# Optimization experiments

Hardware: AMD Instinct MI355X
Metric: run time of the kernel (lower is better)

## Reference

```python
import jax, jax.numpy as jnp
import numpy as np

N_NODES = 100000


def setup_inputs() -> dict:
    key = jax.random.key(0)
    ks = jax.random.split(key, 7)
    feats = jax.random.normal(ks[0], (N_NODES, 128), dtype=jnp.float32)
    src = jax.random.randint(ks[1], (1000000,), 0, N_NODES)
    dst = jax.random.randint(ks[2], (1000000,), 0, N_NODES)
    W1 = jax.random.normal(ks[3], (128, 128), dtype=jnp.float32) * (1.0 / np.sqrt(128))
    b1 = jnp.zeros((128,), dtype=jnp.float32)
    W2 = jax.random.normal(ks[4], (128, 40), dtype=jnp.float32) * (1.0 / np.sqrt(128))
    b2 = jnp.zeros((40,), dtype=jnp.float32)
    return {"feats": feats, "src": src, "dst": dst, "W1": W1, "b1": b1, "W2": W2, "b2": b2}


def _sage_gcn_layer(h, src, dst, deg, W, b):
    # DGL SAGEConv aggregator_type='gcn':
    #   neigh = sum over in-edges of src features; h = (neigh + h_self) / (in_deg + 1); out = h @ W + b
    neigh = jax.ops.segment_sum(h[src], dst, num_segments=N_NODES)  # [N, d]
    agg = (neigh + h) / (deg[:, None] + 1.0)
    return agg @ W + b


def reference(feats, src, dst, W1, b1, W2, b2):
    deg = jax.ops.segment_sum(jnp.ones_like(dst, dtype=feats.dtype), dst, num_segments=N_NODES)
    h1 = jax.nn.relu(_sage_gcn_layer(feats, src, dst, deg, W1, b1))  # dropout = identity (eval)
    h2 = _sage_gcn_layer(h1, src, dst, deg, W2, b2)
    # original returns (h_list, h); h_list = [h1, h2], final h = h2
    return (h1, h2)
```

## Files before the change

kernel.cpp:

```cpp
#include <hip/hip_runtime.h>

static inline int ceil_div(int a, int b){ return (a+b-1)/b; }

__global__ __launch_bounds__(256) void k_hist(const int* __restrict__ dst, int E, int* __restrict__ cnt){
  int e = blockIdx.x*256 + threadIdx.x;
  if (e < E) atomicAdd(&cnt[dst[e]], 1);
}

__global__ __launch_bounds__(256) void k_scan_a(const int* __restrict__ cnt, int N, int* __restrict__ bsum){
  __shared__ int s[256];
  int t = threadIdx.x;
  int i0 = blockIdx.x*512 + 2*t;
  int a = (i0   < N) ? cnt[i0]   : 0;
  int b = (i0+1 < N) ? cnt[i0+1] : 0;
  s[t] = a + b;
  __syncthreads();
  for (int off=128; off>0; off>>=1){ if (t<off) s[t]+=s[t+off]; __syncthreads(); }
  if (t==0) bsum[blockIdx.x] = s[0];
}

__global__ __launch_bounds__(256) void k_scan_b(int* __restrict__ bsum, int nb){
  __shared__ int s[256];
  int t = threadIdx.x;
  int v0=0,v1=0,v2=0,v3=0;
  int i0 = t*4;
  if (i0   < nb) v0 = bsum[i0];
  if (i0+1 < nb) v1 = bsum[i0+1];
  if (i0+2 < nb) v2 = bsum[i0+2];
  if (i0+3 < nb) v3 = bsum[i0+3];
  int tsum = v0+v1+v2+v3;
  s[t] = tsum;
  __syncthreads();
  for (int off=1; off<256; off<<=1){
    int v = (t>=off) ? s[t-off] : 0;
    __syncthreads();
    s[t] += v;
    __syncthreads();
  }
  int excl = s[t] - tsum;
  if (i0   < nb) bsum[i0]   = excl;
  if (i0+1 < nb) bsum[i0+1] = excl + v0;
  if (i0+2 < nb) bsum[i0+2] = excl + v0 + v1;
  if (i0+3 < nb) bsum[i0+3] = excl + v0 + v1 + v2;
}

__global__ __launch_bounds__(256) void k_scan_c(const int* __restrict__ cnt, int N,
                                                const int* __restrict__ bsum, int* __restrict__ offs){
  __shared__ int s[256];
  int t = threadIdx.x;
  int i0 = blockIdx.x*512 + 2*t;
  int a = (i0   < N) ? cnt[i0]   : 0;
  int b = (i0+1 < N) ? cnt[i0+1] : 0;
  int tsum = a+b;
  s[t] = tsum;
  __syncthreads();
  for (int off=1; off<256; off<<=1){
    int v = (t>=off) ? s[t-off] : 0;
    __syncthreads();
    s[t] += v;
    __syncthreads();
  }
  int excl = s[t] - tsum + bsum[blockIdx.x];
  if (i0   < N) offs[i0]   = excl;
  if (i0+1 < N) offs[i0+1] = excl + a;
}

__global__ __launch_bounds__(256) void k_place(const int* __restrict__ src, const int* __restrict__ dst, int E,
                                               int* __restrict__ offs, int* __restrict__ ss){
  int e = blockIdx.x*256 + threadIdx.x;
  if (e < E){
    int d = dst[e];
    int p = atomicAdd(&offs[d], 1);
    ss[p] = src[e];
  }
}

__global__ __launch_bounds__(256) void k_agg1(const float* __restrict__ feats,
    const int* __restrict__ ss, const int* __restrict__ offs, const int* __restrict__ cnt,
    float* __restrict__ aggout, int N){
  int w = (int)((blockIdx.x*256u + threadIdx.x) >> 6);
  int lane = threadIdx.x & 63;
  if (w >= N) return;
  int c   = __builtin_amdgcn_readfirstlane(cnt[w]);
  int beg = __builtin_amdgcn_readfirstlane(offs[w]) - c;
  const float4* f4 = (const float4*)feats;
  int half = lane >> 5;
  int qc   = lane & 31;
  float4 acc = make_float4(0.f,0.f,0.f,0.f);
  int i = 0;
  for (; i+8 <= c; i += 8){
    int i0 = ss[beg+i  +half];
    int i1 = ss[beg+i+2+half];
    int i2 = ss[beg+i+4+half];
    int i3 = ss[beg+i+6+half];
    float4 a = f4[(size_t)i0*32 + qc];
    float4 b = f4[(size_t)i1*32 + qc];
    float4 cc= f4[(size_t)i2*32 + qc];
    float4 d = f4[(size_t)i3*32 + qc];
    acc.x += (a.x + b.x) + (cc.x + d.x);
    acc.y += (a.y + b.y) + (cc.y + d.y);
    acc.z += (a.z + b.z) + (cc.z + d.z);
    acc.w += (a.w + b.w) + (cc.w + d.w);
  }
  for (; i+2 <= c; i += 2){
    int i0 = ss[beg+i+half];
    float4 a = f4[(size_t)i0*32 + qc];
    acc.x += a.x; acc.y += a.y; acc.z += a.z; acc.w += a.w;
  }
  acc.x += __shfl_down(acc.x, 32, 64);
  acc.y += __shfl_down(acc.y, 32, 64);
  acc.z += __shfl_down(acc.z, 32, 64);
  acc.w += __shfl_down(acc.w, 32, 64);
  if (lane < 32){
    if (i < c){
      int i0 = ss[beg+i];
      float4 a = f4[(size_t)i0*32 + qc];
      acc.x += a.x; acc.y += a.y; acc.z += a.z; acc.w += a.w;
    }
    float4 s = f4[(size_t)w*32 + qc];
    float inv = 1.0f / (float)(c + 1);
    float4 o;
    o.x = (acc.x + s.x) * inv;
    o.y = (acc.y + s.y) * inv;
    o.z = (acc.z + s.z) * inv;
    o.w = (acc.w + s.w) * inv;
    ((float4*)aggout)[(size_t)w*32 + qc] = o;
  }
}

__global__ __launch_bounds__(256) void k_gemm12(float* __restrict__ h1,
    const float* __restrict__ W1, const float* __restrict__ b1,
    const float* __restrict__ W2, float* __restrict__ t1, int N){
  __shared__ float sA[64*132];
  __shared__ float sW[5120];
  int t = threadIdx.x;
  int r0 = blockIdx.x*64;
  for (int it=0; it<8; ++it){
    int flat = it*1024 + t*4;
    int r = flat>>7, d = flat&127;
    float4 v = make_float4(0.f,0.f,0.f,0.f);
    if (r0+r < N) v = *(const float4*)(h1 + (size_t)(r0+r)*128 + d);
    *(float4*)&sA[r*132 + d] = v;
  }
  int rg = t>>4, cg = t&15;
  float acc[4][8];
#pragma unroll
  for (int i=0;i<4;++i)
#pragma unroll
    for (int j=0;j<8;++j) acc[i][j]=0.f;

  for (int kc=0; kc<4; ++kc){
    __syncthreads();
#pragma unroll
    for (int it=0; it<4; ++it){
      int flat = it*1024 + t*4;
      *(float4*)&sW[flat] = *(const float4*)(W1 + kc*4096 + flat);
    }
    __syncthreads();
#pragma unroll 4
    for (int dd=0; dd<32; ++dd){
      int d = kc*32 + dd;
      float4 w0 = *(const float4*)&sW[dd*128 + cg*4];
      float4 w1 = *(const float4*)&sW[dd*128 + 64 + cg*4];
      float a0 = sA[(rg   )*132 + d];
      float a1 = sA[(rg+16)*132 + d];
      float a2 = sA[(rg+32)*132 + d];
      float a3 = sA[(rg+48)*132 + d];
      acc[0][0]+=a0*w0.x; acc[0][1]+=a0*w0.y; acc[0][2]+=a0*w0.z; acc[0][3]+=a0*w0.w;
      acc[0][4]+=a0*w1.x; acc[0][5]+=a0*w1.y; acc[0][6]+=a0*w1.z; acc[0][7]+=a0*w1.w;
      acc[1][0]+=a1*w0.x; acc[1][1]+=a1*w0.y; acc[1][2]+=a1*w0.z; acc[1][3]+=a1*w0.w;
      acc[1][4]+=a1*w1.x; acc[1][5]+=a1*w1.y; acc[1][6]+=a1*w1.z; acc[1][7]+=a1*w1.w;
      acc[2][0]+=a2*w0.x; acc[2][1]+=a2*w0.y; acc[2][2]+=a2*w0.z; acc[2][3]+=a2*w0.w;
      acc[2][4]+=a2*w1.x; acc[2][5]+=a2*w1.y; acc[2][6]+=a2*w1.z; acc[2][7]+=a2*w1.w;
      acc[3][0]+=a3*w0.x; acc[3][1]+=a3*w0.y; acc[3][2]+=a3*w0.z; acc[3][3]+=a3*w0.w;
      acc[3][4]+=a3*w1.x; acc[3][5]+=a3*w1.y; acc[3][6]+=a3*w1.z; acc[3][7]+=a3*w1.w;
    }
  }
  __syncthreads();

  float4 bb0 = *(const float4*)(b1 + cg*4);
  float4 bb1 = *(const float4*)(b1 + 64 + cg*4);
#pragma unroll
  for (int i=0;i<4;++i){
    int rr = rg + i*16;
    int r  = r0 + rr;
    float4 o0, o1;
    o0.x = fmaxf(acc[i][0]+bb0.x, 0.f); o0.y = fmaxf(acc[i][1]+bb0.y, 0.f);
    o0.z = fmaxf(acc[i][2]+bb0.z, 0.f); o0.w = fmaxf(acc[i][3]+bb0.w, 0.f);
    o1.x = fmaxf(acc[i][4]+bb1.x, 0.f); o1.y = fmaxf(acc[i][5]+bb1.y, 0.f);
    o1.z = fmaxf(acc[i][6]+bb1.z, 0.f); o1.w = fmaxf(acc[i][7]+bb1.w, 0.f);
    *(float4*)&sA[rr*132 + cg*4]      = o0;
    *(float4*)&sA[rr*132 + 64 + cg*4] = o1;
    if (r < N){
      *(float4*)(h1 + (size_t)r*128 + cg*4)      = o0;
      *(float4*)(h1 + (size_t)r*128 + 64 + cg*4) = o1;
    }
  }
#pragma unroll
  for (int it=0; it<5; ++it){
    int flat = it*1024 + t*4;
    *(float4*)&sW[flat] = *(const float4*)(W2 + flat);
  }
  __syncthreads();

  int rg2 = t>>3, cg2 = t&7;
  float a2c[2][5];
#pragma unroll
  for (int i=0;i<2;++i)
#pragma unroll
    for (int j=0;j<5;++j) a2c[i][j]=0.f;
#pragma unroll 4
  for (int d=0; d<128; ++d){
    float a0 = sA[(rg2   )*132 + d];
    float a1 = sA[(rg2+32)*132 + d];
#pragma unroll
    for (int jj=0;jj<5;++jj){
      float wv = sW[d*40 + cg2 + 8*jj];
      a2c[0][jj] += a0*wv;
      a2c[1][jj] += a1*wv;
    }
  }
#pragma unroll
  for (int i=0;i<2;++i){
    int r = r0 + rg2 + i*32;
    if (r < N){
#pragma unroll
      for (int jj=0;jj<5;++jj) t1[(size_t)r*40 + cg2 + 8*jj] = a2c[i][jj];
    }
  }
}

__global__ __launch_bounds__(256) void k_agg2(const float* __restrict__ t1,
    const int* __restrict__ ss, const int* __restrict__ offs, const int* __restrict__ cnt,
    const float* __restrict__ b2, float* __restrict__ h2, int N){
  int w = (int)((blockIdx.x*256u + threadIdx.x) >> 6);
  int lane = threadIdx.x & 63;
  if (w >= N) return;
  int c   = __builtin_amdgcn_readfirstlane(cnt[w]);
  int beg = __builtin_amdgcn_readfirstlane(offs[w]) - c;
  int l = (lane < 40) ? lane : 0;
  float acc = t1[(size_t)w*40 + l];
  int i = 0;
  for (; i+4 <= c; i += 4){
    int s0 = ss[beg+i], s1 = ss[beg+i+1], s2 = ss[beg+i+2], s3 = ss[beg+i+3];
    float a = t1[(size_t)s0*40 + l];
    float b = t1[(size_t)s1*40 + l];
    float cc= t1[(size_t)s2*40 + l];
    float d = t1[(size_t)s3*40 + l];
    acc += (a + b) + (cc + d);
  }
  for (; i < c; ++i) acc += t1[(size_t)ss[beg+i]*40 + l];
  float inv = 1.0f / (float)(c + 1);
  if (lane < 40) h2[(size_t)w*40 + lane] = acc*inv + b2[lane];
}

extern "C" void kernel_launch(void* const* d_in, const int* in_sizes, int n_in,
                              void* d_out, int out_size, void* d_ws, size_t ws_size,
                              hipStream_t stream){
  const float* feats = (const float*)d_in[0];
  const int*   src   = (const int*)d_in[1];
  const int*   dst   = (const int*)d_in[2];
  const float* W1    = (const float*)d_in[3];
  const float* b1    = (const float*)d_in[4];
  const float* W2    = (const float*)d_in[5];
  const float* b2    = (const float*)d_in[6];
  int N = in_sizes[0] / 128;
  int E = in_sizes[1];
  float* h1 = (float*)d_out;
  float* h2 = h1 + (size_t)N*128;

  size_t need = 0;
  auto lay = [&](size_t bytes)->size_t{ size_t p = need; need += (bytes + 511) & ~(size_t)511; return p; };
  size_t o_cnt    = lay((size_t)N*4);
  size_t o_offs   = lay((size_t)N*4);
  size_t o_bsum   = lay(4096);
  size_t o_ss     = lay((size_t)E*4);
  size_t o_t1     = lay((size_t)N*40*4);
  if (need > ws_size) return;

  char* wp = (char*)d_ws;
  int*   cnt    = (int*)(wp + o_cnt);
  int*   offs   = (int*)(wp + o_offs);
  int*   bsum   = (int*)(wp + o_bsum);
  int*   ss     = (int*)(wp + o_ss);
  float* t1     = (float*)(wp + o_t1);

  hipMemsetAsync(cnt, 0, (size_t)N*4, stream);

  int nb = ceil_div(N, 512);
  k_hist  <<<ceil_div(E,256), 256, 0, stream>>>(dst, E, cnt);
  k_scan_a<<<nb,              256, 0, stream>>>(cnt, N, bsum);
  k_scan_b<<<1,               256, 0, stream>>>(bsum, nb);
  k_scan_c<<<nb,              256, 0, stream>>>(cnt, N, bsum, offs);
  k_place <<<ceil_div(E,256), 256, 0, stream>>>(src, dst, E, offs, ss);

  k_agg1  <<<ceil_div(N,4),   256, 0, stream>>>(feats, ss, offs, cnt, h1, N);
  k_gemm12<<<ceil_div(N,64),  256, 0, stream>>>(h1, W1, b1, W2, t1, N);
  k_agg2  <<<ceil_div(N,4),   256, 0, stream>>>(t1, ss, offs, cnt, b2, h2, N);
}
```

Baseline: 425.0 us.

## Fuse layer-1 aggregation into the GEMM kernel via shared memory

Merges the first gather-aggregation kernel into the dense GEMM kernel. Each block aggregates its 64 rows directly into shared memory with one wave per row using float2 lanes, so the intermediate aggregate no longer makes a round trip through global memory. W2 is also stored transposed in shared memory so the second GEMM can read float4 vectors. The cost is that the gather now runs inside a kernel with heavy shared-memory use and one block per 64 rows, which may lower occupancy and latency hiding for the irregular gathers.

After: 465.4 us. 9.5% more time.

```diff
diff --git a/kernel.cpp b/kernel.cpp
--- a/kernel.cpp
+++ b/kernel.cpp
@@ -75,73 +75,50 @@
   }
 }
 
-__global__ __launch_bounds__(256) void k_agg1(const float* __restrict__ feats,
+__global__ __launch_bounds__(256) void k_fused1(const float* __restrict__ feats,
     const int* __restrict__ ss, const int* __restrict__ offs, const int* __restrict__ cnt,
-    float* __restrict__ aggout, int N){
-  int w = (int)((blockIdx.x*256u + threadIdx.x) >> 6);
-  int lane = threadIdx.x & 63;
-  if (w >= N) return;
-  int c   = __builtin_amdgcn_readfirstlane(cnt[w]);
-  int beg = __builtin_amdgcn_readfirstlane(offs[w]) - c;
-  const float4* f4 = (const float4*)feats;
-  int half = lane >> 5;
-  int qc   = lane & 31;
-  float4 acc = make_float4(0.f,0.f,0.f,0.f);
-  int i = 0;
-  for (; i+8 <= c; i += 8){
-    int i0 = ss[beg+i  +half];
-    int i1 = ss[beg+i+2+half];
-    int i2 = ss[beg+i+4+half];
-    int i3 = ss[beg+i+6+half];
-    float4 a = f4[(size_t)i0*32 + qc];
-    float4 b = f4[(size_t)i1*32 + qc];
-    float4 cc= f4[(size_t)i2*32 + qc];
-    float4 d = f4[(size_t)i3*32 + qc];
-    acc.x += (a.x + b.x) + (cc.x + d.x);
-    acc.y += (a.y + b.y) + (cc.y + d.y);
-    acc.z += (a.z + b.z) + (cc.z + d.z);
-    acc.w += (a.w + b.w) + (cc.w + d.w);
-  }
-  for (; i+2 <= c; i += 2){
-    int i0 = ss[beg+i+half];
-    float4 a = f4[(size_t)i0*32 + qc];
-    acc.x += a.x; acc.y += a.y; acc.z += a.z; acc.w += a.w;
-  }
-  acc.x += __shfl_down(acc.x, 32, 64);
-  acc.y += __shfl_down(acc.y, 32, 64);
-  acc.z += __shfl_down(acc.z, 32, 64);
-  acc.w += __shfl_down(acc.w, 32, 64);
-  if (lane < 32){
-    if (i < c){
-      int i0 = ss[beg+i];
-      float4 a = f4[(size_t)i0*32 + qc];
-      acc.x += a.x; acc.y += a.y; acc.z += a.z; acc.w += a.w;
-    }
-    float4 s = f4[(size_t)w*32 + qc];
-    float inv = 1.0f / (float)(c + 1);
-    float4 o;
-    o.x = (acc.x + s.x) * inv;
-    o.y = (acc.y + s.y) * inv;
-    o.z = (acc.z + s.z) * inv;
-    o.w = (acc.w + s.w) * inv;
-    ((float4*)aggout)[(size_t)w*32 + qc] = o;
-  }
-}
-
-__global__ __launch_bounds__(256) void k_gemm12(float* __restrict__ h1,
     const float* __restrict__ W1, const float* __restrict__ b1,
-    const float* __restrict__ W2, float* __restrict__ t1, int N){
+    const float* __restrict__ W2,
+    float* __restrict__ h1, float* __restrict__ t1, int N){
   __shared__ float sA[64*132];
-  __shared__ float sW[5120];
+  __shared__ float sW[40*132];
   int t = threadIdx.x;
   int r0 = blockIdx.x*64;
-  for (int it=0; it<8; ++it){
-    int flat = it*1024 + t*4;
-    int r = flat>>7, d = flat&127;
-    float4 v = make_float4(0.f,0.f,0.f,0.f);
-    if (r0+r < N) v = *(const float4*)(h1 + (size_t)(r0+r)*128 + d);
-    *(float4*)&sA[r*132 + d] = v;
-  }
+
+  {
+    int wid = t >> 6, lane = t & 63;
+    const float2* f2 = (const float2*)feats;
+    for (int k2=0; k2<16; ++k2){
+      int rr = wid*16 + k2;
+      int w  = r0 + rr;
+      float2 acc = make_float2(0.f, 0.f);
+      if (w < N){
+        int c   = __builtin_amdgcn_readfirstlane(cnt[w]);
+        int beg = __builtin_amdgcn_readfirstlane(offs[w]) - c;
+        acc = f2[(size_t)w*64 + lane];
+        int i = 0;
+        for (; i+8 <= c; i += 8){
+          int s0=ss[beg+i  ], s1=ss[beg+i+1], s2=ss[beg+i+2], s3=ss[beg+i+3];
+          int s4=ss[beg+i+4], s5=ss[beg+i+5], s6=ss[beg+i+6], s7=ss[beg+i+7];
+          float2 a0=f2[(size_t)s0*64+lane], a1=f2[(size_t)s1*64+lane];
+          float2 a2=f2[(size_t)s2*64+lane], a3=f2[(size_t)s3*64+lane];
+          float2 a4=f2[(size_t)s4*64+lane], a5=f2[(size_t)s5*64+lane];
+          float2 a6=f2[(size_t)s6*64+lane], a7=f2[(size_t)s7*64+lane];
+          acc.x += ((a0.x+a1.x)+(a2.x+a3.x)) + ((a4.x+a5.x)+(a6.x+a7.x));
+          acc.y += ((a0.y+a1.y)+(a2.y+a3.y)) + ((a4.y+a5.y)+(a6.y+a7.y));
+        }
+        for (; i < c; ++i){
+          int s0 = ss[beg+i];
+          float2 a = f2[(size_t)s0*64 + lane];
+          acc.x += a.x; acc.y += a.y;
+        }
+        float inv = 1.0f / (float)(c + 1);
+        acc.x *= inv; acc.y *= inv;
+      }
+      *(float2*)&sA[rr*132 + 2*lane] = acc;
+    }
+  }
+
   int rg = t>>4, cg = t&15;
   float acc[4][8];
 #pragma unroll
@@ -199,7 +176,14 @@
 #pragma unroll
   for (int it=0; it<5; ++it){
     int flat = it*1024 + t*4;
-    *(float4*)&sW[flat] = *(const float4*)(W2 + flat);
+    float4 v = *(const float4*)(W2 + flat);
+    const float* vp = (const float*)&v;
+#pragma unroll
+    for (int j=0;j<4;++j){
+      int idx = flat + j;
+      int d = idx / 40, col = idx % 40;
+      sW[col*132 + d] = vp[j];
+    }
   }
   __syncthreads();
 
@@ -209,15 +193,14 @@
   for (int i=0;i<2;++i)
 #pragma unroll
     for (int j=0;j<5;++j) a2c[i][j]=0.f;
-#pragma unroll 4
-  for (int d=0; d<128; ++d){
-    float a0 = sA[(rg2   )*132 + d];
-    float a1 = sA[(rg2+32)*132 + d];
+  for (int d0=0; d0<32; ++d0){
+    float4 a0 = *(const float4*)&sA[(rg2   )*132 + 4*d0];
+    float4 a1 = *(const float4*)&sA[(rg2+32)*132 + 4*d0];
 #pragma unroll
     for (int jj=0;jj<5;++jj){
-      float wv = sW[d*40 + cg2 + 8*jj];
-      a2c[0][jj] += a0*wv;
-      a2c[1][jj] += a1*wv;
+      float4 wv = *(const float4*)&sW[(cg2+8*jj)*132 + 4*d0];
+      a2c[0][jj] += a0.x*wv.x + a0.y*wv.y + a0.z*wv.z + a0.w*wv.w;
+      a2c[1][jj] += a1.x*wv.x + a1.y*wv.y + a1.z*wv.z + a1.w*wv.w;
     }
   }
 #pragma unroll
@@ -294,7 +277,6 @@
   k_scan_c<<<nb,              256, 0, stream>>>(cnt, N, bsum, offs);
   k_place <<<ceil_div(E,256), 256, 0, stream>>>(src, dst, E, offs, ss);
 
-  k_agg1  <<<ceil_div(N,4),   256, 0, stream>>>(feats, ss, offs, cnt, h1, N);
-  k_gemm12<<<ceil_div(N,64),  256, 0, stream>>>(h1, W1, b1, W2, t1, N);
+  k_fused1<<<ceil_div(N,64),  256, 0, stream>>>(feats, ss, offs, cnt, W1, b1, W2, h1, t1, N);
   k_agg2  <<<ceil_div(N,4),   256, 0, stream>>>(t1, ss, offs, cnt, b2, h2, N);
 }
```
